# Performance work log

Hardware: AMD Instinct MI355X
Metric: run time of the kernel (lower is better)

## Reference

```python
import jax, jax.numpy as jnp
import numpy as np


def setup_inputs() -> dict:
    key = jax.random.key(0)
    B, S, D = 4, 8192, 768
    x = jax.random.normal(key, (B, S, D), dtype=jnp.float32)
    return {"x": x}


def reference(x) -> jnp.ndarray:
    # FNet mixing: FFT along seq axis, then FFT along hidden axis, take real part.
    # Equivalent to the original nested map_fn(tf.signal.fft) over transposed slices.
    g = jnp.fft.fft2(x.astype(jnp.complex64), axes=(1, 2))  # [B, S, D] complex64
    return jnp.real(g)
```

## Files before the change

kernel.cpp:

```cpp
#include <hip/hip_runtime.h>
#include <math.h>


#define S_LEN 8192
#define D_LEN 768
#define NK2 33
#define ROWS_PB (128 * NK2)
#define TWO_PI 6.28318530717958647692f

__device__ __forceinline__ int dr128(int p) {
    return ((p & 1) << 6) | (((p >> 1) & 3) << 4) | (((p >> 3) & 3) << 2) | (p >> 5);
}
__device__ __forceinline__ int dr256(int p) {
    return ((p & 3) << 6) | (((p >> 2) & 3) << 4) | (((p >> 4) & 3) << 2) | (p >> 6);
}
__device__ __forceinline__ int F2(int pos) {
    return 4 * pos + (pos >> 2);
}

__device__ __forceinline__ float2 cadd(float2 a, float2 b) {
    return make_float2(a.x + b.x, a.y + b.y);
}
__device__ __forceinline__ float2 csub(float2 a, float2 b) {
    return make_float2(a.x - b.x, a.y - b.y);
}
__device__ __forceinline__ float2 cmulf(float2 a, float2 b) {
    return make_float2(a.x * b.x - a.y * b.y, a.x * b.y + a.y * b.x);
}
__device__ __forceinline__ float2 mul_mi(float2 a) {
    return make_float2(a.y, -a.x);
}

__device__ __forceinline__ void fft8(const float2* a, float2* X) {
    const float R2 = 0.70710678118654752440f;
    float2 u0 = cadd(a[0], a[4]), v0 = csub(a[0], a[4]);
    float2 u1 = cadd(a[1], a[5]), v1 = csub(a[1], a[5]);
    float2 u2 = cadd(a[2], a[6]), v2 = csub(a[2], a[6]);
    float2 u3 = cadd(a[3], a[7]), v3 = csub(a[3], a[7]);
    v1 = make_float2(R2 * (v1.x + v1.y), R2 * (v1.y - v1.x));
    v2 = mul_mi(v2);
    v3 = make_float2(R2 * (v3.y - v3.x), -R2 * (v3.x + v3.y));
    float2 e0 = cadd(u0, u2), o0 = csub(u0, u2);
    float2 e1 = cadd(u1, u3), o1 = mul_mi(csub(u1, u3));
    X[0] = cadd(e0, e1); X[4] = csub(e0, e1);
    X[2] = cadd(o0, o1); X[6] = csub(o0, o1);
    float2 f0 = cadd(v0, v2), p0 = csub(v0, v2);
    float2 f1 = cadd(v1, v3), p1 = mul_mi(csub(v1, v3));
    X[1] = cadd(f0, f1); X[5] = csub(f0, f1);
    X[3] = cadd(p0, p1); X[7] = csub(p0, p1);
}

#define BFLY4(zre, zim, a0, a1, a2, a3, w1, w2, w3)                            \
    {                                                                          \
        float ar = zre[a0], ai = zim[a0], br = zre[a1], bi = zim[a1];          \
        float cr = zre[a2], ci = zim[a2], er = zre[a3], ei = zim[a3];          \
        float t0r = ar + cr, t0i = ai + ci, t1r = ar - cr, t1i = ai - ci;      \
        float t2r = br + er, t2i = bi + ei, t3r = br - er, t3i = bi - ei;      \
        zre[a0] = t0r + t2r; zim[a0] = t0i + t2i;                              \
        float B1r = t1r + t3i, B1i = t1i - t3r;                                \
        zre[a1] = B1r * w1.x - B1i * w1.y; zim[a1] = B1r * w1.y + B1i * w1.x;  \
        float B2r = t0r - t2r, B2i = t0i - t2i;                                \
        zre[a2] = B2r * w2.x - B2i * w2.y; zim[a2] = B2r * w2.y + B2i * w2.x;  \
        float B3r = t1r - t3i, B3i = t1i + t3r;                                \
        zre[a3] = B3r * w3.x - B3i * w3.y; zim[a3] = B3r * w3.y + B3i * w3.x;  \
    }

__global__ __launch_bounds__(256) void fft_s1_kernel(const float* __restrict__ x,
                                                     float2* __restrict__ Y,
                                                     int b0) {
    __shared__ float2 Z[64 * 33];
    const int bid = blockIdx.x;
    const int dt = bid % 12;
    const int n1 = (bid / 12) % 128;
    const int bb = bid / (12 * 128);
    const int b = b0 + bb;
    const int t = threadIdx.x;
    const int c = t & 31;
    const int na = t >> 5;

    float2 v[8];
    const size_t xbase = ((size_t)b * S_LEN + n1 + 128 * na) * D_LEN + dt * 64 + 2 * c;
    #pragma unroll
    for (int nb2 = 0; nb2 < 8; ++nb2) {
        v[nb2] = *(const float2*)(x + xbase + (size_t)nb2 * 1024 * D_LEN);
    }

    float2 g[8];
    fft8(v, g);

    {
        float s, co;
        sincosf(-TWO_PI * (float)na / 64.0f, &s, &co);
        const float2 w = make_float2(co, s);
        float2 wk = w;
        #pragma unroll
        for (int k = 1; k < 8; ++k) {
            g[k] = cmulf(g[k], wk);
            wk = cmulf(wk, w);
        }
    }

    #pragma unroll
    for (int k = 0; k < 8; ++k) Z[(8 * k + na) * 33 + c] = g[k];
    __syncthreads();

    float2 h[8], r[8];
    #pragma unroll
    for (int j = 0; j < 8; ++j) h[j] = Z[(8 * na + j) * 33 + c];
    fft8(h, r);
    __syncthreads();
    #pragma unroll
    for (int ka = 0; ka < 8; ++ka) Z[(na + 8 * ka) * 33 + c] = r[ka];
    __syncthreads();

    const size_t rcb = (size_t)bb * ROWS_PB + (size_t)n1 * NK2;
    #pragma unroll
    for (int it = 0; it < 5; ++it) {
        const int k2 = na + 8 * it;
        if (k2 <= 32) {
            const float2 z1 = Z[k2 * 33 + c];
            const float2 z2 = Z[((64 - k2) & 63) * 33 + c];
            const float Ar = 0.5f * (z1.x + z2.x), Ai = 0.5f * (z1.y - z2.y);
            const float Br = 0.5f * (z1.y + z2.y), Bi = -0.5f * (z1.x - z2.x);
            const size_t idx = (rcb + k2) * D_LEN + dt * 64 + 2 * c;
            *(float4*)(Y + idx) = make_float4(Ar, Ai, Br, Bi);
        }
    }
}

__global__ __launch_bounds__(256) void fft_s2_kernel(float2* __restrict__ Y) {
    __shared__ float sre[128 * 32], sim[128 * 32];
    __shared__ float2 pt[128];
    __shared__ float2 t128[128];
    const int bid = blockIdx.x;
    const int dt = bid % 24;
    const int k2 = (bid / 24) % NK2;
    const int bb = bid / (24 * NK2);
    const int t = threadIdx.x;
    const int d = t & 31;
    const int g = t >> 5;

    if (t < 128) {
        float s, co;
        sincosf(-TWO_PI * (float)(t * k2) / 8192.0f, &s, &co);
        pt[t] = make_float2(co, s);
        sincosf(-TWO_PI * (float)t / 128.0f, &s, &co);
        t128[t] = make_float2(co, s);
    }
    __syncthreads();

    const size_t base_rc = (size_t)bb * ROWS_PB + k2;
    const int col = dt * 32 + d;
    for (int j = g; j < 128; j += 8) {
        const float2 v = Y[(base_rc + (size_t)j * NK2) * D_LEN + col];
        const float2 w = pt[j];
        sre[j * 32 + d] = v.x * w.x - v.y * w.y;
        sim[j * 32 + d] = v.x * w.y + v.y * w.x;
    }
    __syncthreads();

    #pragma unroll
    for (int it = 0; it < 4; ++it) {
        const int p = g + 8 * it;
        const int a0 = p * 32 + d;
        const float2 w1 = t128[p], w2 = t128[2 * p], w3 = t128[3 * p];
        BFLY4(sre, sim, a0, a0 + 32 * 32, a0 + 64 * 32, a0 + 96 * 32, w1, w2, w3);
    }
    __syncthreads();
    #pragma unroll
    for (int it = 0; it < 4; ++it) {
        const int i = g + 8 * it;
        const int blk = i >> 3, p = i & 7;
        const int a0 = (blk * 32 + p) * 32 + d;
        const float2 w1 = t128[4 * p], w2 = t128[8 * p], w3 = t128[12 * p];
        BFLY4(sre, sim, a0, a0 + 8 * 32, a0 + 16 * 32, a0 + 24 * 32, w1, w2, w3);
    }
    __syncthreads();
    #pragma unroll
    for (int it = 0; it < 4; ++it) {
        const int i = g + 8 * it;
        const int blk = i >> 1, p = i & 1;
        const int a0 = (blk * 8 + p) * 32 + d;
        const float2 w1 = t128[16 * p], w2 = t128[32 * p], w3 = t128[48 * p];
        BFLY4(sre, sim, a0, a0 + 2 * 32, a0 + 4 * 32, a0 + 6 * 32, w1, w2, w3);
    }
    __syncthreads();
    #pragma unroll
    for (int it = 0; it < 8; ++it) {
        const int i = g + 8 * it;
        const int a0 = (2 * i) * 32 + d, a1 = a0 + 32;
        float ar = sre[a0], ai = sim[a0], br = sre[a1], bi = sim[a1];
        sre[a0] = ar + br; sim[a0] = ai + bi;
        sre[a1] = ar - br; sim[a1] = ai - bi;
    }
    __syncthreads();

    for (int j = g; j < 128; j += 8) {
        const int k1 = dr128(j);
        Y[(base_rc + (size_t)k1 * NK2) * D_LEN + col] =
            make_float2(sre[j * 32 + d], sim[j * 32 + d]);
    }
}

__global__ __launch_bounds__(256) void fft_d_kernel(const float2* __restrict__ Y,
                                                    float* __restrict__ out,
                                                    int b0) {
    __shared__ float sre[6528], sim[6528];
    __shared__ float2 t768[256];
    const int t = threadIdx.x;
    const int rc0 = blockIdx.x * 8;

    {
        float s, co;
        sincosf(-TWO_PI * (float)t / 768.0f, &s, &co);
        t768[t] = make_float2(co, s);
    }

    {
        const int rw = t >> 5;
        const int q = t & 31;
        const size_t grow = (size_t)(rc0 + rw) * D_LEN;
        #pragma unroll
        for (int jl = 0; jl < 24; ++jl) {
            const int n = q + 32 * jl;
            const float2 v = Y[grow + n];
            const int pos = (n % 3) * 256 + n / 3;
            const int fi = 8 * pos + 2 * (pos >> 2) + rw;
            sre[fi] = v.x;
            sim[fi] = v.y;
        }
    }
    __syncthreads();

    const int m = t & 3;
    const int q2 = t >> 2;
    float2* s2re = (float2*)sre;
    float2* s2im = (float2*)sim;

#define BFLY4V(a0, a1, a2, a3, w1, w2, w3)                                      \
    {                                                                           \
        float2 ar = s2re[a0], ai = s2im[a0], br = s2re[a1], bi = s2im[a1];      \
        float2 cr = s2re[a2], ci = s2im[a2], er = s2re[a3], ei = s2im[a3];      \
        float2 t0r = make_float2(ar.x + cr.x, ar.y + cr.y);                     \
        float2 t0i = make_float2(ai.x + ci.x, ai.y + ci.y);                     \
        float2 t1r = make_float2(ar.x - cr.x, ar.y - cr.y);                     \
        float2 t1i = make_float2(ai.x - ci.x, ai.y - ci.y);                     \
        float2 t2r = make_float2(br.x + er.x, br.y + er.y);                     \
        float2 t2i = make_float2(bi.x + ei.x, bi.y + ei.y);                     \
        float2 t3r = make_float2(br.x - er.x, br.y - er.y);                     \
        float2 t3i = make_float2(bi.x - ei.x, bi.y - ei.y);                     \
        s2re[a0] = make_float2(t0r.x + t2r.x, t0r.y + t2r.y);                   \
        s2im[a0] = make_float2(t0i.x + t2i.x, t0i.y + t2i.y);                   \
        float2 B1r = make_float2(t1r.x + t3i.x, t1r.y + t3i.y);                 \
        float2 B1i = make_float2(t1i.x - t3r.x, t1i.y - t3r.y);                 \
        s2re[a1] = make_float2(B1r.x * w1.x - B1i.x * w1.y,                     \
                               B1r.y * w1.x - B1i.y * w1.y);                    \
        s2im[a1] = make_float2(B1r.x * w1.y + B1i.x * w1.x,                     \
                               B1r.y * w1.y + B1i.y * w1.x);                    \
        float2 B2r = make_float2(t0r.x - t2r.x, t0r.y - t2r.y);                 \
        float2 B2i = make_float2(t0i.x - t2i.x, t0i.y - t2i.y);                 \
        s2re[a2] = make_float2(B2r.x * w2.x - B2i.x * w2.y,                     \
                               B2r.y * w2.x - B2i.y * w2.y);                    \
        s2im[a2] = make_float2(B2r.x * w2.y + B2i.x * w2.x,                     \
                               B2r.y * w2.y + B2i.y * w2.x);                    \
        float2 B3r = make_float2(t1r.x - t3i.x, t1r.y - t3i.y);                 \
        float2 B3i = make_float2(t1i.x + t3r.x, t1i.y + t3r.y);                 \
        s2re[a3] = make_float2(B3r.x * w3.x - B3i.x * w3.y,                     \
                               B3r.y * w3.x - B3i.y * w3.y);                    \
        s2im[a3] = make_float2(B3r.x * w3.y + B3i.x * w3.x,                     \
                               B3r.y * w3.y + B3i.y * w3.x);                    \
    }
#define CSQ(w) make_float2((w).x * (w).x - (w).y * (w).y, 2.0f * (w).x * (w).y)
#define CMU(a, b) make_float2((a).x * (b).x - (a).y * (b).y,                    \
                              (a).x * (b).y + (a).y * (b).x)

    #pragma unroll
    for (int jj = 0; jj < 3; ++jj) {
        const int bf = q2 + 64 * jj;
        const int sub = bf >> 6;
        const int p = bf & 63;
        const int base = sub * 256 + p;
        const float2 w1 = t768[3 * p];
        const float2 w2 = CSQ(w1);
        const float2 w3 = CMU(w1, w2);
        BFLY4V(F2(base) + m, F2(base + 64) + m, F2(base + 128) + m,
               F2(base + 192) + m, w1, w2, w3);
    }
    __syncthreads();
    #pragma unroll
    for (int jj = 0; jj < 3; ++jj) {
        const int bf = q2 + 64 * jj;
        const int sub = bf >> 6;
        const int i = bf & 63;
        const int blk = i >> 4, p = i & 15;
        const int base = sub * 256 + blk * 64 + p;
        const float2 w1 = t768[12 * p];
        const float2 w2 = CSQ(w1);
        const float2 w3 = CMU(w1, w2);
        BFLY4V(F2(base) + m, F2(base + 16) + m, F2(base + 32) + m,
               F2(base + 48) + m, w1, w2, w3);
    }
    __syncthreads();
    #pragma unroll
    for (int jj = 0; jj < 3; ++jj) {
        const int bf = q2 + 64 * jj;
        const int sub = bf >> 6;
        const int i = bf & 63;
        const int blk = i >> 2, p = i & 3;
        const int base = sub * 256 + blk * 16 + p;
        const float2 w1 = t768[48 * p];
        const float2 w2 = CSQ(w1);
        const float2 w3 = CMU(w1, w2);
        BFLY4V(F2(base) + m, F2(base + 4) + m, F2(base + 8) + m,
               F2(base + 12) + m, w1, w2, w3);
    }
    __syncthreads();
    {
        const float2 wid = make_float2(1.0f, 0.0f);
        #pragma unroll
        for (int jj = 0; jj < 3; ++jj) {
            const int bf = q2 + 64 * jj;
            const int sub = bf >> 6;
            const int i = bf & 63;
            const int base = sub * 256 + 4 * i;
            BFLY4V(F2(base) + m, F2(base + 1) + m, F2(base + 2) + m,
                   F2(base + 3) + m, wid, wid, wid);
        }
    }
    __syncthreads();

    size_t obase[8], mbase[8];
    bool domir[8];
    #pragma unroll
    for (int rr = 0; rr < 8; ++rr) {
        const int rc = rc0 + rr;
        const int bb = rc / ROWS_PB;
        const int qq = rc - bb * ROWS_PB;
        const int K1 = qq / NK2;
        const int K2 = qq - K1 * NK2;
        const int srow = 64 * K1 + K2;
        const size_t bs = (size_t)(b0 + bb) * S_LEN;
        obase[rr] = (bs + srow) * D_LEN;
        mbase[rr] = (bs + (S_LEN - srow)) * D_LEN;
        domir[rr] = (K2 >= 1 && K2 <= 31);
    }

    const float W3r = -0.5f, W3i = -0.86602540378443864676f;
    const int kk = t;
    const int j8 = dr256(kk);
    const int e0 = F2(j8), e1 = F2(256 + j8), e2 = F2(512 + j8);
    const float2 w = t768[kk];
    const float c1 = w.x, s1 = w.y;
    const float c2 = c1 * c1 - s1 * s1, s2_ = 2.0f * c1 * s1;
    const int md0 = (kk == 0) ? 0 : (768 - kk);
    #pragma unroll
    for (int i2 = 0; i2 < 4; ++i2) {
        const float2 u0r = s2re[e0 + i2], u0i = s2im[e0 + i2];
        const float2 u1r = s2re[e1 + i2], u1i = s2im[e1 + i2];
        const float2 u2r = s2re[e2 + i2], u2i = s2im[e2 + i2];
        const float2 v1r = make_float2(u1r.x * c1 - u1i.x * s1, u1r.y * c1 - u1i.y * s1);
        const float2 v1i = make_float2(u1r.x * s1 + u1i.x * c1, u1r.y * s1 + u1i.y * c1);
        const float2 v2r = make_float2(u2r.x * c2 - u2i.x * s2_, u2r.y * c2 - u2i.y * s2_);
        const float2 v2i = make_float2(u2r.x * s2_ + u2i.x * c2, u2r.y * s2_ + u2i.y * c2);
        const float2 y0 = make_float2(u0r.x + v1r.x + v2r.x, u0r.y + v1r.y + v2r.y);
        const float2 y1 = make_float2(
            u0r.x + (v1r.x * W3r - v1i.x * W3i) + (v2r.x * W3r + v2i.x * W3i),
            u0r.y + (v1r.y * W3r - v1i.y * W3i) + (v2r.y * W3r + v2i.y * W3i));
        const float2 y2 = make_float2(
            u0r.x + (v1r.x * W3r + v1i.x * W3i) + (v2r.x * W3r - v2i.x * W3i),
            u0r.y + (v1r.y * W3r + v1i.y * W3i) + (v2r.y * W3r - v2i.y * W3i));
        #pragma unroll
        for (int h = 0; h < 2; ++h) {
            const int rr = 2 * i2 + h;
            const float v0 = h ? y0.y : y0.x;
            const float v1 = h ? y1.y : y1.x;
            const float v2 = h ? y2.y : y2.x;
            out[obase[rr] + kk] = v0;
            out[obase[rr] + 256 + kk] = v1;
            out[obase[rr] + 512 + kk] = v2;
            if (domir[rr]) {
                out[mbase[rr] + md0] = v0;
                out[mbase[rr] + 512 - kk] = v1;
                out[mbase[rr] + 256 - kk] = v2;
            }
        }
    }
#undef BFLY4V
#undef CSQ
#undef CMU
}

extern "C" void kernel_launch(void* const* d_in, const int* in_sizes, int n_in,
                              void* d_out, int out_size, void* d_ws, size_t ws_size,
                              hipStream_t stream) {
    const float* x = (const float*)d_in[0];
    float* out = (float*)d_out;
    float2* Y = (float2*)d_ws;

    const size_t full_plane_bytes = (size_t)4 * ROWS_PB * D_LEN * sizeof(float2);
    const size_t half_plane_bytes = full_plane_bytes / 2;
    int nb;
    if (ws_size >= full_plane_bytes) nb = 4;
    else if (ws_size >= half_plane_bytes) nb = 2;
    else return;

    for (int b0 = 0; b0 < 4; b0 += nb) {
        fft_s1_kernel<<<dim3(nb * 128 * 12), dim3(256), 0, stream>>>(x, Y, b0);
        fft_s2_kernel<<<dim3(nb * NK2 * 24), dim3(256), 0, stream>>>(Y);
        fft_d_kernel<<<dim3(nb * ROWS_PB / 8), dim3(256), 0, stream>>>(Y, out, b0);
    }
}
```

Before: 122.8 us.

## Widen s1 FFT blocks to 1024 threads covering full hidden row

The first sequence-FFT stage now uses 1024-thread blocks, each handling a whole 768-wide hidden row slab in three 256-column passes, instead of 12 separate 256-thread blocks per n1. Each thread issues all 24 global loads up front to expose more memory-level parallelism, and the twiddle powers are computed once and reused across the passes. The shared tile grows to a 129-element stride. In exchange the grid shrinks by 12x (512 blocks for a full batch), register pressure rises, and extra barriers serialize the three passes.

```diff
diff --git a/kernel.cpp b/kernel.cpp
--- a/kernel.cpp
+++ b/kernel.cpp
@@ -65,65 +65,82 @@
         zre[a3] = B3r * w3.x - B3i * w3.y; zim[a3] = B3r * w3.y + B3i * w3.x;  \
     }
 
-__global__ __launch_bounds__(256) void fft_s1_kernel(const float* __restrict__ x,
-                                                     float2* __restrict__ Y,
-                                                     int b0) {
-    __shared__ float2 Z[64 * 33];
+#define ZSTR2 129
+__global__ __launch_bounds__(1024) void fft_s1_kernel(const float* __restrict__ x,
+                                                      float2* __restrict__ Y,
+                                                      int b0) {
+    __shared__ float2 Z[64 * ZSTR2];
     const int bid = blockIdx.x;
-    const int dt = bid % 12;
-    const int n1 = (bid / 12) % 128;
-    const int bb = bid / (12 * 128);
+    const int n1 = bid % 128;
+    const int bb = bid / 128;
     const int b = b0 + bb;
     const int t = threadIdx.x;
-    const int c = t & 31;
-    const int na = t >> 5;
-
-    float2 v[8];
-    const size_t xbase = ((size_t)b * S_LEN + n1 + 128 * na) * D_LEN + dt * 64 + 2 * c;
-    #pragma unroll
-    for (int nb2 = 0; nb2 < 8; ++nb2) {
-        v[nb2] = *(const float2*)(x + xbase + (size_t)nb2 * 1024 * D_LEN);
-    }
-
-    float2 g[8];
-    fft8(v, g);
-
+    const int c = t & 127;
+    const int na = t >> 7;
+
+    float2 v0[8], v1[8], v2g[8];
     {
-        float s, co;
-        sincosf(-TWO_PI * (float)na / 64.0f, &s, &co);
-        const float2 w = make_float2(co, s);
-        float2 wk = w;
-        #pragma unroll
-        for (int k = 1; k < 8; ++k) {
-            g[k] = cmulf(g[k], wk);
-            wk = cmulf(wk, w);
-        }
-    }
-
-    #pragma unroll
-    for (int k = 0; k < 8; ++k) Z[(8 * k + na) * 33 + c] = g[k];
-    __syncthreads();
-
-    float2 h[8], r[8];
-    #pragma unroll
-    for (int j = 0; j < 8; ++j) h[j] = Z[(8 * na + j) * 33 + c];
-    fft8(h, r);
-    __syncthreads();
-    #pragma unroll
-    for (int ka = 0; ka < 8; ++ka) Z[(na + 8 * ka) * 33 + c] = r[ka];
-    __syncthreads();
+        const size_t rowstep = (size_t)1024 * D_LEN;
+        const size_t xbase =
+            ((size_t)b * S_LEN + n1 + 128 * na) * D_LEN + 2 * c;
+        #pragma unroll
+        for (int nb2 = 0; nb2 < 8; ++nb2)
+            v0[nb2] = *(const float2*)(x + xbase + (size_t)nb2 * rowstep);
+        #pragma unroll
+        for (int nb2 = 0; nb2 < 8; ++nb2)
+            v1[nb2] = *(const float2*)(x + xbase + (size_t)nb2 * rowstep + 256);
+        #pragma unroll
+        for (int nb2 = 0; nb2 < 8; ++nb2)
+            v2g[nb2] = *(const float2*)(x + xbase + (size_t)nb2 * rowstep + 512);
+    }
+
+    float2 wk1, wk2, wk3, wk4, wk5, wk6, wk7;
+    {
+        float s_, co;
+        sincosf(-TWO_PI * (float)na / 64.0f, &s_, &co);
+        wk1 = make_float2(co, s_);
+        wk2 = cmulf(wk1, wk1); wk3 = cmulf(wk2, wk1); wk4 = cmulf(wk3, wk1);
+        wk5 = cmulf(wk4, wk1); wk6 = cmulf(wk5, wk1); wk7 = cmulf(wk6, wk1);
+    }
 
     const size_t rcb = (size_t)bb * ROWS_PB + (size_t)n1 * NK2;
-    #pragma unroll
-    for (int it = 0; it < 5; ++it) {
-        const int k2 = na + 8 * it;
-        if (k2 <= 32) {
-            const float2 z1 = Z[k2 * 33 + c];
-            const float2 z2 = Z[((64 - k2) & 63) * 33 + c];
-            const float Ar = 0.5f * (z1.x + z2.x), Ai = 0.5f * (z1.y - z2.y);
-            const float Br = 0.5f * (z1.y + z2.y), Bi = -0.5f * (z1.x - z2.x);
-            const size_t idx = (rcb + k2) * D_LEN + dt * 64 + 2 * c;
-            *(float4*)(Y + idx) = make_float4(Ar, Ai, Br, Bi);
+
+    #pragma unroll
+    for (int m = 0; m < 3; ++m) {
+        float2 g[8];
+        if (m == 0) fft8(v0, g);
+        else if (m == 1) fft8(v1, g);
+        else fft8(v2g, g);
+        g[1] = cmulf(g[1], wk1); g[2] = cmulf(g[2], wk2);
+        g[3] = cmulf(g[3], wk3); g[4] = cmulf(g[4], wk4);
+        g[5] = cmulf(g[5], wk5); g[6] = cmulf(g[6], wk6);
+        g[7] = cmulf(g[7], wk7);
+
+        if (m > 0) __syncthreads();
+        #pragma unroll
+        for (int k = 0; k < 8; ++k) Z[(8 * k + na) * ZSTR2 + c] = g[k];
+        __syncthreads();
+
+        float2 h[8], r[8];
+        #pragma unroll
+        for (int j = 0; j < 8; ++j) h[j] = Z[(8 * na + j) * ZSTR2 + c];
+        fft8(h, r);
+        __syncthreads();
+        #pragma unroll
+        for (int ka = 0; ka < 8; ++ka) Z[(na + 8 * ka) * ZSTR2 + c] = r[ka];
+        __syncthreads();
+
+        #pragma unroll
+        for (int it = 0; it < 5; ++it) {
+            const int k2 = na + 8 * it;
+            if (k2 <= 32) {
+                const float2 z1 = Z[k2 * ZSTR2 + c];
+                const float2 z2 = Z[((64 - k2) & 63) * ZSTR2 + c];
+                const float Ar = 0.5f * (z1.x + z2.x), Ai = 0.5f * (z1.y - z2.y);
+                const float Br = 0.5f * (z1.y + z2.y), Bi = -0.5f * (z1.x - z2.x);
+                const size_t idx = (rcb + k2) * D_LEN + m * 256 + 2 * c;
+                *(float4*)(Y + idx) = make_float4(Ar, Ai, Br, Bi);
+            }
         }
     }
 }
@@ -405,7 +422,7 @@
     else return;
 
     for (int b0 = 0; b0 < 4; b0 += nb) {
-        fft_s1_kernel<<<dim3(nb * 128 * 12), dim3(256), 0, stream>>>(x, Y, b0);
+        fft_s1_kernel<<<dim3(nb * 128), dim3(1024), 0, stream>>>(x, Y, b0);
         fft_s2_kernel<<<dim3(nb * NK2 * 24), dim3(256), 0, stream>>>(Y);
         fft_d_kernel<<<dim3(nb * ROWS_PB / 8), dim3(256), 0, stream>>>(Y, out, b0);
     }
```

Measured after the change: 131.7 us. 1.07x slower.

## Reorder FFT to hidden axis first with half-spectrum and bf16 intermediates

Applied to the files above, without the earlier changes.

The pipeline is restructured so the 768-point hidden-axis FFT runs first on the real input. Only the non-redundant half spectrum (385 columns) is kept, packed as bf16 complex pairs. Two sequence-axis passes follow, also using bf16 intermediates. The last pass writes the real part with non-temporal stores and fills the conjugate-symmetric half by mirroring. This cuts workspace traffic roughly in half, but bf16 storage of intermediate spectra may degrade accuracy beyond tolerance.

```diff
diff --git a/kernel.cpp b/kernel.cpp
--- a/kernel.cpp
+++ b/kernel.cpp
@@ -4,9 +4,21 @@
 
 #define S_LEN 8192
 #define D_LEN 768
-#define NK2 33
-#define ROWS_PB (128 * NK2)
+#define NKD 385
+#define ZCOLS 388
 #define TWO_PI 6.28318530717958647692f
+
+__device__ __forceinline__ unsigned bf16_of(float f) {
+    unsigned u = __float_as_uint(f);
+    return (u + 0x7FFFu + ((u >> 16) & 1u)) >> 16;
+}
+__device__ __forceinline__ unsigned pack_bf2(float re, float im) {
+    return bf16_of(re) | (bf16_of(im) << 16);
+}
+__device__ __forceinline__ float2 unpack_bf2(unsigned p) {
+    return make_float2(__uint_as_float((p & 0xFFFFu) << 16),
+                       __uint_as_float((p >> 16) << 16));
+}
 
 __device__ __forceinline__ int dr128(int p) {
     return ((p & 1) << 6) | (((p >> 1) & 3) << 4) | (((p >> 3) & 3) << 2) | (p >> 5);
@@ -65,150 +77,12 @@
         zre[a3] = B3r * w3.x - B3i * w3.y; zim[a3] = B3r * w3.y + B3i * w3.x;  \
     }
 
-__global__ __launch_bounds__(256) void fft_s1_kernel(const float* __restrict__ x,
-                                                     float2* __restrict__ Y,
-                                                     int b0) {
-    __shared__ float2 Z[64 * 33];
-    const int bid = blockIdx.x;
-    const int dt = bid % 12;
-    const int n1 = (bid / 12) % 128;
-    const int bb = bid / (12 * 128);
-    const int b = b0 + bb;
-    const int t = threadIdx.x;
-    const int c = t & 31;
-    const int na = t >> 5;
-
-    float2 v[8];
-    const size_t xbase = ((size_t)b * S_LEN + n1 + 128 * na) * D_LEN + dt * 64 + 2 * c;
-    #pragma unroll
-    for (int nb2 = 0; nb2 < 8; ++nb2) {
-        v[nb2] = *(const float2*)(x + xbase + (size_t)nb2 * 1024 * D_LEN);
-    }
-
-    float2 g[8];
-    fft8(v, g);
-
-    {
-        float s, co;
-        sincosf(-TWO_PI * (float)na / 64.0f, &s, &co);
-        const float2 w = make_float2(co, s);
-        float2 wk = w;
-        #pragma unroll
-        for (int k = 1; k < 8; ++k) {
-            g[k] = cmulf(g[k], wk);
-            wk = cmulf(wk, w);
-        }
-    }
-
-    #pragma unroll
-    for (int k = 0; k < 8; ++k) Z[(8 * k + na) * 33 + c] = g[k];
-    __syncthreads();
-
-    float2 h[8], r[8];
-    #pragma unroll
-    for (int j = 0; j < 8; ++j) h[j] = Z[(8 * na + j) * 33 + c];
-    fft8(h, r);
-    __syncthreads();
-    #pragma unroll
-    for (int ka = 0; ka < 8; ++ka) Z[(na + 8 * ka) * 33 + c] = r[ka];
-    __syncthreads();
-
-    const size_t rcb = (size_t)bb * ROWS_PB + (size_t)n1 * NK2;
-    #pragma unroll
-    for (int it = 0; it < 5; ++it) {
-        const int k2 = na + 8 * it;
-        if (k2 <= 32) {
-            const float2 z1 = Z[k2 * 33 + c];
-            const float2 z2 = Z[((64 - k2) & 63) * 33 + c];
-            const float Ar = 0.5f * (z1.x + z2.x), Ai = 0.5f * (z1.y - z2.y);
-            const float Br = 0.5f * (z1.y + z2.y), Bi = -0.5f * (z1.x - z2.x);
-            const size_t idx = (rcb + k2) * D_LEN + dt * 64 + 2 * c;
-            *(float4*)(Y + idx) = make_float4(Ar, Ai, Br, Bi);
-        }
-    }
-}
-
-__global__ __launch_bounds__(256) void fft_s2_kernel(float2* __restrict__ Y) {
-    __shared__ float sre[128 * 32], sim[128 * 32];
-    __shared__ float2 pt[128];
-    __shared__ float2 t128[128];
-    const int bid = blockIdx.x;
-    const int dt = bid % 24;
-    const int k2 = (bid / 24) % NK2;
-    const int bb = bid / (24 * NK2);
-    const int t = threadIdx.x;
-    const int d = t & 31;
-    const int g = t >> 5;
-
-    if (t < 128) {
-        float s, co;
-        sincosf(-TWO_PI * (float)(t * k2) / 8192.0f, &s, &co);
-        pt[t] = make_float2(co, s);
-        sincosf(-TWO_PI * (float)t / 128.0f, &s, &co);
-        t128[t] = make_float2(co, s);
-    }
-    __syncthreads();
-
-    const size_t base_rc = (size_t)bb * ROWS_PB + k2;
-    const int col = dt * 32 + d;
-    for (int j = g; j < 128; j += 8) {
-        const float2 v = Y[(base_rc + (size_t)j * NK2) * D_LEN + col];
-        const float2 w = pt[j];
-        sre[j * 32 + d] = v.x * w.x - v.y * w.y;
-        sim[j * 32 + d] = v.x * w.y + v.y * w.x;
-    }
-    __syncthreads();
-
-    #pragma unroll
-    for (int it = 0; it < 4; ++it) {
-        const int p = g + 8 * it;
-        const int a0 = p * 32 + d;
-        const float2 w1 = t128[p], w2 = t128[2 * p], w3 = t128[3 * p];
-        BFLY4(sre, sim, a0, a0 + 32 * 32, a0 + 64 * 32, a0 + 96 * 32, w1, w2, w3);
-    }
-    __syncthreads();
-    #pragma unroll
-    for (int it = 0; it < 4; ++it) {
-        const int i = g + 8 * it;
-        const int blk = i >> 3, p = i & 7;
-        const int a0 = (blk * 32 + p) * 32 + d;
-        const float2 w1 = t128[4 * p], w2 = t128[8 * p], w3 = t128[12 * p];
-        BFLY4(sre, sim, a0, a0 + 8 * 32, a0 + 16 * 32, a0 + 24 * 32, w1, w2, w3);
-    }
-    __syncthreads();
-    #pragma unroll
-    for (int it = 0; it < 4; ++it) {
-        const int i = g + 8 * it;
-        const int blk = i >> 1, p = i & 1;
-        const int a0 = (blk * 8 + p) * 32 + d;
-        const float2 w1 = t128[16 * p], w2 = t128[32 * p], w3 = t128[48 * p];
-        BFLY4(sre, sim, a0, a0 + 2 * 32, a0 + 4 * 32, a0 + 6 * 32, w1, w2, w3);
-    }
-    __syncthreads();
-    #pragma unroll
-    for (int it = 0; it < 8; ++it) {
-        const int i = g + 8 * it;
-        const int a0 = (2 * i) * 32 + d, a1 = a0 + 32;
-        float ar = sre[a0], ai = sim[a0], br = sre[a1], bi = sim[a1];
-        sre[a0] = ar + br; sim[a0] = ai + bi;
-        sre[a1] = ar - br; sim[a1] = ai - bi;
-    }
-    __syncthreads();
-
-    for (int j = g; j < 128; j += 8) {
-        const int k1 = dr128(j);
-        Y[(base_rc + (size_t)k1 * NK2) * D_LEN + col] =
-            make_float2(sre[j * 32 + d], sim[j * 32 + d]);
-    }
-}
-
-__global__ __launch_bounds__(256) void fft_d_kernel(const float2* __restrict__ Y,
-                                                    float* __restrict__ out,
-                                                    int b0) {
+__global__ __launch_bounds__(256) void kd_kernel(const float* __restrict__ x,
+                                                 unsigned* __restrict__ Zp) {
     __shared__ float sre[6528], sim[6528];
     __shared__ float2 t768[256];
     const int t = threadIdx.x;
-    const int rc0 = blockIdx.x * 8;
+    const size_t r0 = (size_t)blockIdx.x * 8;
 
     {
         float s, co;
@@ -219,15 +93,18 @@
     {
         const int rw = t >> 5;
         const int q = t & 31;
-        const size_t grow = (size_t)(rc0 + rw) * D_LEN;
-        #pragma unroll
-        for (int jl = 0; jl < 24; ++jl) {
-            const int n = q + 32 * jl;
-            const float2 v = Y[grow + n];
-            const int pos = (n % 3) * 256 + n / 3;
-            const int fi = 8 * pos + 2 * (pos >> 2) + rw;
-            sre[fi] = v.x;
-            sim[fi] = v.y;
+        const float* xrow = x + (r0 + rw) * D_LEN;
+        #pragma unroll
+        for (int jl = 0; jl < 12; ++jl) {
+            const int n = 2 * (q + 32 * jl);
+            const float2 v = *(const float2*)(xrow + n);
+            const int pa = (n % 3) * 256 + n / 3;
+            const int fa = 8 * pa + 2 * (pa >> 2) + rw;
+            sre[fa] = v.x; sim[fa] = 0.0f;
+            const int nb1 = n + 1;
+            const int pb = (nb1 % 3) * 256 + nb1 / 3;
+            const int fb = 8 * pb + 2 * (pb >> 2) + rw;
+            sre[fb] = v.y; sim[fb] = 0.0f;
         }
     }
     __syncthreads();
@@ -329,22 +206,6 @@
     }
     __syncthreads();
 
-    size_t obase[8], mbase[8];
-    bool domir[8];
-    #pragma unroll
-    for (int rr = 0; rr < 8; ++rr) {
-        const int rc = rc0 + rr;
-        const int bb = rc / ROWS_PB;
-        const int qq = rc - bb * ROWS_PB;
-        const int K1 = qq / NK2;
-        const int K2 = qq - K1 * NK2;
-        const int srow = 64 * K1 + K2;
-        const size_t bs = (size_t)(b0 + bb) * S_LEN;
-        obase[rr] = (bs + srow) * D_LEN;
-        mbase[rr] = (bs + (S_LEN - srow)) * D_LEN;
-        domir[rr] = (K2 >= 1 && K2 <= 31);
-    }
-
     const float W3r = -0.5f, W3i = -0.86602540378443864676f;
     const int kk = t;
     const int j8 = dr256(kk);
@@ -352,7 +213,6 @@
     const float2 w = t768[kk];
     const float c1 = w.x, s1 = w.y;
     const float c2 = c1 * c1 - s1 * s1, s2_ = 2.0f * c1 * s1;
-    const int md0 = (kk == 0) ? 0 : (768 - kk);
     #pragma unroll
     for (int i2 = 0; i2 < 4; ++i2) {
         const float2 u0r = s2re[e0 + i2], u0i = s2im[e0 + i2];
@@ -362,32 +222,171 @@
         const float2 v1i = make_float2(u1r.x * s1 + u1i.x * c1, u1r.y * s1 + u1i.y * c1);
         const float2 v2r = make_float2(u2r.x * c2 - u2i.x * s2_, u2r.y * c2 - u2i.y * s2_);
         const float2 v2i = make_float2(u2r.x * s2_ + u2i.x * c2, u2r.y * s2_ + u2i.y * c2);
-        const float2 y0 = make_float2(u0r.x + v1r.x + v2r.x, u0r.y + v1r.y + v2r.y);
-        const float2 y1 = make_float2(
-            u0r.x + (v1r.x * W3r - v1i.x * W3i) + (v2r.x * W3r + v2i.x * W3i),
-            u0r.y + (v1r.y * W3r - v1i.y * W3i) + (v2r.y * W3r + v2i.y * W3i));
-        const float2 y2 = make_float2(
-            u0r.x + (v1r.x * W3r + v1i.x * W3i) + (v2r.x * W3r - v2i.x * W3i),
-            u0r.y + (v1r.y * W3r + v1i.y * W3i) + (v2r.y * W3r - v2i.y * W3i));
+        const float2 y0r = make_float2(u0r.x + v1r.x + v2r.x, u0r.y + v1r.y + v2r.y);
+        const float2 y0i = make_float2(u0i.x + v1i.x + v2i.x, u0i.y + v1i.y + v2i.y);
+        const float2 y1r = make_float2(
+            u0r.x + W3r * (v1r.x + v2r.x) + W3i * (v2i.x - v1i.x),
+            u0r.y + W3r * (v1r.y + v2r.y) + W3i * (v2i.y - v1i.y));
+        const float2 y1i = make_float2(
+            u0i.x + W3i * (v1r.x - v2r.x) + W3r * (v1i.x + v2i.x),
+            u0i.y + W3i * (v1r.y - v2r.y) + W3r * (v1i.y + v2i.y));
         #pragma unroll
         for (int h = 0; h < 2; ++h) {
-            const int rr = 2 * i2 + h;
-            const float v0 = h ? y0.y : y0.x;
-            const float v1 = h ? y1.y : y1.x;
-            const float v2 = h ? y2.y : y2.x;
-            out[obase[rr] + kk] = v0;
-            out[obase[rr] + 256 + kk] = v1;
-            out[obase[rr] + 512 + kk] = v2;
-            if (domir[rr]) {
-                out[mbase[rr] + md0] = v0;
-                out[mbase[rr] + 512 - kk] = v1;
-                out[mbase[rr] + 256 - kk] = v2;
+            unsigned* zrow = Zp + (r0 + 2 * i2 + h) * ZCOLS;
+            const float a0r = h ? y0r.y : y0r.x, a0i = h ? y0i.y : y0i.x;
+            zrow[kk] = pack_bf2(a0r, a0i);
+            if (kk <= 128) {
+                const float a1r = h ? y1r.y : y1r.x, a1i = h ? y1i.y : y1i.x;
+                zrow[256 + kk] = pack_bf2(a1r, a1i);
             }
         }
     }
 #undef BFLY4V
 #undef CSQ
 #undef CMU
+}
+
+__global__ __launch_bounds__(256) void ks1_kernel(const unsigned* __restrict__ Zp,
+                                                  unsigned* __restrict__ Up) {
+    __shared__ float2 Z[64 * 33];
+    const int bid = blockIdx.x;
+    const int ct = bid % 13;
+    const int n1 = (bid / 13) % 128;
+    const int bb = bid / (13 * 128);
+    const int t = threadIdx.x;
+    const int c = t & 31;
+    const int na = t >> 5;
+    const int col = ct * 32 + c;
+    const bool ok = (col < NKD);
+
+    float2 v[8];
+    if (ok) {
+        const size_t rbase =
+            ((size_t)bb * S_LEN + n1 + 128 * na) * ZCOLS + col;
+        #pragma unroll
+        for (int nb2 = 0; nb2 < 8; ++nb2)
+            v[nb2] = unpack_bf2(Zp[rbase + (size_t)nb2 * 1024 * ZCOLS]);
+    } else {
+        #pragma unroll
+        for (int nb2 = 0; nb2 < 8; ++nb2) v[nb2] = make_float2(0.f, 0.f);
+    }
+
+    float2 g[8];
+    fft8(v, g);
+    {
+        float s_, co;
+        sincosf(-TWO_PI * (float)na / 64.0f, &s_, &co);
+        const float2 w = make_float2(co, s_);
+        float2 wk = w;
+        #pragma unroll
+        for (int k = 1; k < 8; ++k) {
+            g[k] = cmulf(g[k], wk);
+            wk = cmulf(wk, w);
+        }
+    }
+    #pragma unroll
+    for (int k = 0; k < 8; ++k) Z[(8 * k + na) * 33 + c] = g[k];
+    __syncthreads();
+
+    float2 h[8], r[8];
+    #pragma unroll
+    for (int j = 0; j < 8; ++j) h[j] = Z[(8 * na + j) * 33 + c];
+    fft8(h, r);
+
+    if (ok) {
+        const size_t ubase = ((size_t)bb * S_LEN + 64 * n1 + na) * ZCOLS + col;
+        #pragma unroll
+        for (int ka = 0; ka < 8; ++ka)
+            Up[ubase + (size_t)ka * 8 * ZCOLS] = pack_bf2(r[ka].x, r[ka].y);
+    }
+}
+
+__global__ __launch_bounds__(256) void ks2_kernel(const unsigned* __restrict__ Up,
+                                                  float* __restrict__ out,
+                                                  int b0) {
+    __shared__ float sre[128 * 32], sim[128 * 32];
+    __shared__ float2 pt[128];
+    __shared__ float2 t128[128];
+    const int bid = blockIdx.x;
+    const int ct = bid % 13;
+    const int k2 = (bid / 13) % 64;
+    const int bb = bid / (13 * 64);
+    const int t = threadIdx.x;
+    const int d = t & 31;
+    const int g = t >> 5;
+    const int col = ct * 32 + d;
+    const bool ok = (col < NKD);
+
+    if (t < 128) {
+        float s, co;
+        sincosf(-TWO_PI * (float)(t * k2) / 8192.0f, &s, &co);
+        pt[t] = make_float2(co, s);
+        sincosf(-TWO_PI * (float)t / 128.0f, &s, &co);
+        t128[t] = make_float2(co, s);
+    }
+    __syncthreads();
+
+    const size_t ubase = ((size_t)bb * S_LEN + k2) * ZCOLS + col;
+    for (int j = g; j < 128; j += 8) {
+        float2 v = make_float2(0.f, 0.f);
+        if (ok) v = unpack_bf2(Up[ubase + (size_t)j * 64 * ZCOLS]);
+        const float2 w = pt[j];
+        sre[j * 32 + d] = v.x * w.x - v.y * w.y;
+        sim[j * 32 + d] = v.x * w.y + v.y * w.x;
+    }
+    __syncthreads();
+
+    #pragma unroll
+    for (int it = 0; it < 4; ++it) {
+        const int p = g + 8 * it;
+        const int a0 = p * 32 + d;
+        const float2 w1 = t128[p], w2 = t128[2 * p], w3 = t128[3 * p];
+        BFLY4(sre, sim, a0, a0 + 32 * 32, a0 + 64 * 32, a0 + 96 * 32, w1, w2, w3);
+    }
+    __syncthreads();
+    #pragma unroll
+    for (int it = 0; it < 4; ++it) {
+        const int i = g + 8 * it;
+        const int blk = i >> 3, p = i & 7;
+        const int a0 = (blk * 32 + p) * 32 + d;
+        const float2 w1 = t128[4 * p], w2 = t128[8 * p], w3 = t128[12 * p];
+        BFLY4(sre, sim, a0, a0 + 8 * 32, a0 + 16 * 32, a0 + 24 * 32, w1, w2, w3);
+    }
+    __syncthreads();
+    #pragma unroll
+    for (int it = 0; it < 4; ++it) {
+        const int i = g + 8 * it;
+        const int blk = i >> 1, p = i & 1;
+        const int a0 = (blk * 8 + p) * 32 + d;
+        const float2 w1 = t128[16 * p], w2 = t128[32 * p], w3 = t128[48 * p];
+        BFLY4(sre, sim, a0, a0 + 2 * 32, a0 + 4 * 32, a0 + 6 * 32, w1, w2, w3);
+    }
+    __syncthreads();
+    #pragma unroll
+    for (int it = 0; it < 8; ++it) {
+        const int i = g + 8 * it;
+        const int a0 = (2 * i) * 32 + d, a1 = a0 + 32;
+        float ar = sre[a0], ai = sim[a0], br = sre[a1], bi = sim[a1];
+        sre[a0] = ar + br; sim[a0] = ai + bi;
+        sre[a1] = ar - br; sim[a1] = ai - bi;
+    }
+    __syncthreads();
+
+    if (ok) {
+        const size_t obase = (size_t)(b0 + bb) * S_LEN * D_LEN;
+        const bool mir = (col >= 1 && col <= 383);
+        for (int j = g; j < 128; j += 8) {
+            const int k1 = dr128(j);
+            const int ks = k2 + 64 * k1;
+            const float re = sre[j * 32 + d];
+            __builtin_nontemporal_store(re, &out[obase + (size_t)ks * D_LEN + col]);
+            if (mir) {
+                const int ms = (S_LEN - ks) & (S_LEN - 1);
+                __builtin_nontemporal_store(
+                    re, &out[obase + (size_t)ms * D_LEN + (D_LEN - col)]);
+            }
+        }
+    }
 }
 
 extern "C" void kernel_launch(void* const* d_in, const int* in_sizes, int n_in,
@@ -395,18 +394,21 @@
                               hipStream_t stream) {
     const float* x = (const float*)d_in[0];
     float* out = (float*)d_out;
-    float2* Y = (float2*)d_ws;
-
-    const size_t full_plane_bytes = (size_t)4 * ROWS_PB * D_LEN * sizeof(float2);
-    const size_t half_plane_bytes = full_plane_bytes / 2;
+
+    const size_t plane_full = (size_t)4 * S_LEN * ZCOLS;
     int nb;
-    if (ws_size >= full_plane_bytes) nb = 4;
-    else if (ws_size >= half_plane_bytes) nb = 2;
+    if (ws_size >= 2 * plane_full * sizeof(unsigned)) nb = 4;
+    else if (ws_size >= plane_full * sizeof(unsigned)) nb = 2;
     else return;
 
+    const size_t plane_u = (size_t)nb * S_LEN * ZCOLS;
+    unsigned* Zp = (unsigned*)d_ws;
+    unsigned* Up = Zp + plane_u;
+
     for (int b0 = 0; b0 < 4; b0 += nb) {
-        fft_s1_kernel<<<dim3(nb * 128 * 12), dim3(256), 0, stream>>>(x, Y, b0);
-        fft_s2_kernel<<<dim3(nb * NK2 * 24), dim3(256), 0, stream>>>(Y);
-        fft_d_kernel<<<dim3(nb * ROWS_PB / 8), dim3(256), 0, stream>>>(Y, out, b0);
-    }
-}
+        kd_kernel<<<dim3(nb * S_LEN / 8), dim3(256), 0, stream>>>(
+            x + (size_t)b0 * S_LEN * D_LEN, Zp);
+        ks1_kernel<<<dim3(nb * 128 * 13), dim3(256), 0, stream>>>(Zp, Up);
+        ks2_kernel<<<dim3(nb * 64 * 13), dim3(256), 0, stream>>>(Up, out, b0);
+    }
+}
```

New measurement: 172.2 us. +40.3%, slower.
